# Kernel optimization log

Measured on AMD Instinct MI355X. Metric: run time of the kernel, lower is better.

## Reference

```python
import jax, jax.numpy as jnp
import numpy as np

B, S, H = 32, 512, 256
NUM_BINS = 256
MAX_LEN = 4096  # static pad length = S * max_duration (8); original pads to data-dependent max

def _quantize(values, num_bins, v_min, v_max):
    # torch.bucketize(right=False) == searchsorted side='left' on linspace boundaries
    v = jnp.clip(values, v_min, v_max)
    boundaries = jnp.linspace(v_min, v_max, num_bins)
    bins = jnp.searchsorted(boundaries, v, side='left')
    return jnp.clip(bins, 0, num_bins - 1)

def _length_regulate(x, duration_target):
    # x: [B,S,H]; durations rounded, clamped >=1
    dur = jnp.maximum(jnp.round(duration_target).astype(jnp.int32), 1)  # [B,S]
    cum = jnp.cumsum(dur, axis=1)                                       # [B,S]
    t = jnp.arange(MAX_LEN)                                             # [T]
    # frame t belongs to token j where cum[j-1] <= t < cum[j]
    idx = jax.vmap(lambda c: jnp.searchsorted(c, t, side='right'))(cum)  # [B,T]
    valid = (t[None, :] < cum[:, -1:]).astype(x.dtype)                   # [B,T]
    idx = jnp.clip(idx, 0, S - 1)
    out = jnp.take_along_axis(x, idx[..., None], axis=1)                 # [B,T,H]
    return out * valid[..., None]

def setup_inputs() -> dict:
    key = jax.random.key(0)
    k = jax.random.split(key, 6)
    return {
        'encoder_output': jax.random.normal(k[0], (B, S, H), jnp.float32),
        'pitch_target': 50.0 + 350.0 * jax.random.uniform(k[1], (B, S), jnp.float32),
        'energy_target': jax.random.uniform(k[2], (B, S), jnp.float32),
        'duration_target': 1.0 + 7.0 * jax.random.uniform(k[3], (B, S), jnp.float32),
        'pitch_table': 0.02 * jax.random.normal(k[4], (NUM_BINS, H), jnp.float32),
        'energy_table': 0.02 * jax.random.normal(k[5], (NUM_BINS, H), jnp.float32),
    }

def reference(encoder_output, pitch_target, energy_target, duration_target,
              pitch_table, energy_table):
    # dropout is identity in eval mode
    pitch_bins = _quantize(pitch_target, NUM_BINS, 50.0, 400.0)
    energy_bins = _quantize(energy_target, NUM_BINS, 0.0, 1.0)
    out = encoder_output + pitch_table[pitch_bins] + energy_table[energy_bins]
    return _length_regulate(out, duration_target)
```

## Files before the change

kernel.cpp:

```cpp
#include <hip/hip_runtime.h>

#define BB 32
#define SS 512
#define HH 256
#define NBINS 256
#define TMAX 4096

__device__ __forceinline__ double boundary(int i, double vmin, double vmax, double step) {
    if (i == NBINS - 1) return vmax;
    return (double)i * step + vmin;
}

__device__ __forceinline__ int quantize_bin(float v, float vminf, float vmaxf) {
    v = fminf(fmaxf(v, vminf), vmaxf);
    double vd = (double)v;
    double vmin = (double)vminf, vmax = (double)vmaxf;
    double step = (vmax - vmin) / (double)(NBINS - 1);
    int g = (int)ceil((vd - vmin) / step);
    g = max(0, min(NBINS - 1, g));
    while (g > 0 && vd <= boundary(g - 1, vmin, vmax, step)) g--;
    while (g < NBINS - 1 && vd > boundary(g, vmin, vmax, step)) g++;
    return g;
}

__global__ __launch_bounds__(512)
void prep_kernel(const float* __restrict__ pitch,
                 const float* __restrict__ energy,
                 const float* __restrict__ dur,
                 int* __restrict__ idx_map,
                 int* __restrict__ pbins,
                 int* __restrict__ ebins) {
    int b = blockIdx.x;
    int s = threadIdx.x;
    __shared__ int cum[SS];

    int tok = b * SS + s;
    pbins[tok] = quantize_bin(pitch[tok], 50.0f, 400.0f);
    ebins[tok] = quantize_bin(energy[tok], 0.0f, 1.0f);
    int d = (int)rintf(dur[tok]);
    if (d < 1) d = 1;
    cum[s] = d;
    __syncthreads();

    for (int off = 1; off < SS; off <<= 1) {
        int add = (s >= off) ? cum[s - off] : 0;
        __syncthreads();
        cum[s] += add;
        __syncthreads();
    }
    int total = cum[SS - 1];

    for (int t = s; t < TMAX; t += SS) {
        int j;
        if (t >= total) {
            j = -1;
        } else {
            int lo = 0, hi = SS;
            while (lo < hi) {
                int m = (lo + hi) >> 1;
                if (cum[m] <= t) lo = m + 1; else hi = m;
            }
            j = (lo > SS - 1) ? (SS - 1) : lo;
        }
        idx_map[b * TMAX + t] = j;
    }
}

__global__ __launch_bounds__(256)
void gather_kernel(const float* __restrict__ enc,
                   const float* __restrict__ ptab,
                   const float* __restrict__ etab,
                   const int* __restrict__ idx_map,
                   const int* __restrict__ pbins,
                   const int* __restrict__ ebins,
                   float* __restrict__ out) {
    int row = blockIdx.x * 4 + (threadIdx.x >> 6);
    int lane = threadIdx.x & 63;
    int b = row >> 12;
    int j = idx_map[row];

    float4* outv = reinterpret_cast<float4*>(out + (size_t)row * HH) + lane;
    if (j < 0) {
        *outv = make_float4(0.f, 0.f, 0.f, 0.f);
        return;
    }
    int tok = b * SS + j;
    int pb = pbins[tok];
    int eb = ebins[tok];
    const float4 e = reinterpret_cast<const float4*>(enc  + (size_t)tok * HH)[lane];
    const float4 p = reinterpret_cast<const float4*>(ptab + (size_t)pb  * HH)[lane];
    const float4 q = reinterpret_cast<const float4*>(etab + (size_t)eb  * HH)[lane];
    float4 r;
    r.x = (e.x + p.x) + q.x;
    r.y = (e.y + p.y) + q.y;
    r.z = (e.z + p.z) + q.z;
    r.w = (e.w + p.w) + q.w;
    *outv = r;
}

extern "C" void kernel_launch(void* const* d_in, const int* in_sizes, int n_in,
                              void* d_out, int out_size, void* d_ws, size_t ws_size,
                              hipStream_t stream) {
    const float* enc    = (const float*)d_in[0];
    const float* pitch  = (const float*)d_in[1];
    const float* energy = (const float*)d_in[2];
    const float* dur    = (const float*)d_in[3];
    const float* ptab   = (const float*)d_in[4];
    const float* etab   = (const float*)d_in[5];
    float* out = (float*)d_out;

    char* ws = (char*)d_ws;
    int* idx_map = (int*)ws;
    int* pbins   = (int*)(ws + (size_t)BB * TMAX * 4);
    int* ebins   = pbins + BB * SS;

    prep_kernel<<<BB, SS, 0, stream>>>(pitch, energy, dur, idx_map, pbins, ebins);

    int rows = BB * TMAX;
    gather_kernel<<<rows / 4, 256, 0, stream>>>(enc, ptab, etab, idx_map, pbins, ebins, out);
}
```

Baseline: 174.6 us.

## Pack token and bin indices into one map; process 16 rows per wave reusing values

The prep kernel now packs the token index, pitch bin and energy bin into a single int per output frame, so the gather no longer does dependent loads from separate bin arrays. Each wave now writes 16 consecutive output rows. It shuffles the packed indices across lanes and reloads and recomputes the encoder and table sum only when the token changes, because consecutive frames often repeat a token. This cuts redundant reads and index loads but reduces the number of waves and serializes the stores within a wave.

```diff
diff --git a/kernel.cpp b/kernel.cpp
--- a/kernel.cpp
+++ b/kernel.cpp
@@ -5,6 +5,7 @@
 #define HH 256
 #define NBINS 256
 #define TMAX 4096
+#define ROWS_PER_WAVE 16
 
 __device__ __forceinline__ double boundary(int i, double vmin, double vmax, double step) {
     if (i == NBINS - 1) return vmax;
@@ -27,16 +28,16 @@
 void prep_kernel(const float* __restrict__ pitch,
                  const float* __restrict__ energy,
                  const float* __restrict__ dur,
-                 int* __restrict__ idx_map,
-                 int* __restrict__ pbins,
-                 int* __restrict__ ebins) {
+                 int* __restrict__ map) {
     int b = blockIdx.x;
     int s = threadIdx.x;
     __shared__ int cum[SS];
+    __shared__ int pb_sh[SS];
+    __shared__ int eb_sh[SS];
 
     int tok = b * SS + s;
-    pbins[tok] = quantize_bin(pitch[tok], 50.0f, 400.0f);
-    ebins[tok] = quantize_bin(energy[tok], 0.0f, 1.0f);
+    pb_sh[s] = quantize_bin(pitch[tok], 50.0f, 400.0f);
+    eb_sh[s] = quantize_bin(energy[tok], 0.0f, 1.0f);
     int d = (int)rintf(dur[tok]);
     if (d < 1) d = 1;
     cum[s] = d;
@@ -51,18 +52,19 @@
     int total = cum[SS - 1];
 
     for (int t = s; t < TMAX; t += SS) {
-        int j;
+        int packed;
         if (t >= total) {
-            j = -1;
+            packed = -1;
         } else {
             int lo = 0, hi = SS;
             while (lo < hi) {
                 int m = (lo + hi) >> 1;
                 if (cum[m] <= t) lo = m + 1; else hi = m;
             }
-            j = (lo > SS - 1) ? (SS - 1) : lo;
+            int j = (lo > SS - 1) ? (SS - 1) : lo;
+            packed = j | (pb_sh[j] << 9) | (eb_sh[j] << 17);
         }
-        idx_map[b * TMAX + t] = j;
+        map[b * TMAX + t] = packed;
     }
 }
 
@@ -70,32 +72,42 @@
 void gather_kernel(const float* __restrict__ enc,
                    const float* __restrict__ ptab,
                    const float* __restrict__ etab,
-                   const int* __restrict__ idx_map,
-                   const int* __restrict__ pbins,
-                   const int* __restrict__ ebins,
+                   const int* __restrict__ map,
                    float* __restrict__ out) {
-    int row = blockIdx.x * 4 + (threadIdx.x >> 6);
+    int wave = blockIdx.x * 4 + (threadIdx.x >> 6);
     int lane = threadIdx.x & 63;
-    int b = row >> 12;
-    int j = idx_map[row];
+    int row0 = wave * ROWS_PER_WAVE;
+    int b = row0 >> 12;
 
-    float4* outv = reinterpret_cast<float4*>(out + (size_t)row * HH) + lane;
-    if (j < 0) {
-        *outv = make_float4(0.f, 0.f, 0.f, 0.f);
-        return;
+    int my_packed = (lane < ROWS_PER_WAVE) ? map[row0 + lane] : 0;
+
+    int last_packed = -2;
+    float4 val = make_float4(0.f, 0.f, 0.f, 0.f);
+    float4* outv = reinterpret_cast<float4*>(out + (size_t)row0 * HH) + lane;
+
+    #pragma unroll
+    for (int r = 0; r < ROWS_PER_WAVE; ++r) {
+        int packed = __shfl(my_packed, r);
+        if (packed != last_packed) {
+            if (packed < 0) {
+                val = make_float4(0.f, 0.f, 0.f, 0.f);
+            } else {
+                int j  = packed & 511;
+                int pb = (packed >> 9) & 255;
+                int eb = (packed >> 17) & 255;
+                int tok = b * SS + j;
+                const float4 e = reinterpret_cast<const float4*>(enc  + (size_t)tok * HH)[lane];
+                const float4 p = reinterpret_cast<const float4*>(ptab + (size_t)pb  * HH)[lane];
+                const float4 q = reinterpret_cast<const float4*>(etab + (size_t)eb  * HH)[lane];
+                val.x = (e.x + p.x) + q.x;
+                val.y = (e.y + p.y) + q.y;
+                val.z = (e.z + p.z) + q.z;
+                val.w = (e.w + p.w) + q.w;
+            }
+            last_packed = packed;
+        }
+        outv[(size_t)r * (HH / 4)] = val;
     }
-    int tok = b * SS + j;
-    int pb = pbins[tok];
-    int eb = ebins[tok];
-    const float4 e = reinterpret_cast<const float4*>(enc  + (size_t)tok * HH)[lane];
-    const float4 p = reinterpret_cast<const float4*>(ptab + (size_t)pb  * HH)[lane];
-    const float4 q = reinterpret_cast<const float4*>(etab + (size_t)eb  * HH)[lane];
-    float4 r;
-    r.x = (e.x + p.x) + q.x;
-    r.y = (e.y + p.y) + q.y;
-    r.z = (e.z + p.z) + q.z;
-    r.w = (e.w + p.w) + q.w;
-    *outv = r;
 }
 
 extern "C" void kernel_launch(void* const* d_in, const int* in_sizes, int n_in,
@@ -109,13 +121,10 @@
     const float* etab   = (const float*)d_in[5];
     float* out = (float*)d_out;
 
-    char* ws = (char*)d_ws;
-    int* idx_map = (int*)ws;
-    int* pbins   = (int*)(ws + (size_t)BB * TMAX * 4);
-    int* ebins   = pbins + BB * SS;
+    int* map = (int*)d_ws;
 
-    prep_kernel<<<BB, SS, 0, stream>>>(pitch, energy, dur, idx_map, pbins, ebins);
+    prep_kernel<<<BB, SS, 0, stream>>>(pitch, energy, dur, map);
 
-    int rows = BB * TMAX;
-    gather_kernel<<<rows / 4, 256, 0, stream>>>(enc, ptab, etab, idx_map, pbins, ebins, out);
+    int waves = (BB * TMAX) / ROWS_PER_WAVE;
+    gather_kernel<<<waves / 4, 256, 0, stream>>>(enc, ptab, etab, map, out);
 }
```

After: 173.4 us. About the same (-0.7%).
